# Kernel optimization log

Measured on AMD Instinct MI355X. Metric: run time of the kernel, lower is better.

The kernel has to match this reference:

```python
import jax, jax.numpy as jnp
import numpy as np

B, T, D, E, FF, K = 4, 1024, 1024, 8, 2048, 2
SINKHORN_ITERS = 3


def setup_inputs() -> dict:
    key = jax.random.key(0)
    ks = jax.random.split(key, 7)
    scale = 0.02
    return {
        "x": jax.random.normal(ks[0], (B, T, D), dtype=jnp.float32),
        "router_w": jax.random.normal(ks[1], (E, D), dtype=jnp.float32) * scale,  # nn.Linear(D,E).weight
        "router_b": jnp.zeros((E,), dtype=jnp.float32),
        "temperature": jnp.ones((1,), dtype=jnp.float32) * 0.5,
        "wg": jax.random.normal(ks[2], (E, D, FF), dtype=jnp.float32) * scale,   # expert gate weights
        "wp": jax.random.normal(ks[3], (E, D, FF), dtype=jnp.float32) * scale,   # expert proj weights
        "wo": jax.random.normal(ks[4], (E, FF, D), dtype=jnp.float32) * scale,   # expert out_proj weights
    }


def _sinkhorn(log_alpha, iters=SINKHORN_ITERS):
    for _ in range(iters):
        log_alpha = log_alpha - jax.nn.logsumexp(log_alpha, axis=-1, keepdims=True)
        log_alpha = log_alpha - jax.nn.logsumexp(log_alpha, axis=-2, keepdims=True)
    gates = jnp.exp(log_alpha)
    return gates / (jnp.sum(gates, axis=-1, keepdims=True) + 1e-8)


def reference(x, router_w, router_b, temperature, wg, wp, wo):
    # Router scores with clamped temperature (clamp(min=0.1))
    temp = jnp.maximum(temperature, 0.1)
    scores = (jnp.einsum("btd,ed->bte", x, router_w) + router_b) / temp  # [B,T,E]

    # T>1 and E>1 -> Sinkhorn doubly-stochastic normalization
    gates = _sinkhorn(scores)

    topk_vals, topk_idx = jax.lax.top_k(gates, K)                 # [B,T,K]
    topk_gates = topk_vals / (jnp.sum(topk_vals, axis=-1, keepdims=True) + 1e-8)

    # Dense all-expert FFN (relu-gated GLU), matching mask-and-sum semantics.
    # sum_k sum_i (idx_k==i)*gate_k*expert_i(x) == sum_k gate_k * expert_{idx_k}(x)
    g = jax.nn.relu(jnp.einsum("btd,edf->btef", x, wg))           # [B,T,E,FF]
    p = jnp.einsum("btd,edf->btef", x, wp)                        # [B,T,E,FF]
    all_out = jnp.einsum("btef,efd->bted", g * p, wo)             # [B,T,E,D]

    gathered = jnp.take_along_axis(all_out, topk_idx[..., None], axis=2)  # [B,T,K,D]
    expert_out = jnp.sum(gathered * topk_gates[..., None], axis=2)        # [B,T,D]

    return x + expert_out
```

## Files before the change

kernel.cpp:

```cpp
#include <hip/hip_runtime.h>
#include <hip/hip_bf16.h>
#include <stdint.h>

#define B_   4
#define T_   1024
#define D_   1024
#define E_   8
#define FF_  2048
#define NT_  4096
#define LCAP 9216
#define NT1  (D_ / 32)
#define NT2  (FF_ / 32)

typedef unsigned short u16;
typedef __attribute__((ext_vector_type(8))) short bf16x8;
typedef __attribute__((ext_vector_type(4))) float f32x4;

#define MFMA16(a, b, c) __builtin_amdgcn_mfma_f32_16x16x32_bf16((a), (b), (c), 0, 0, 0)

__device__ __forceinline__ u16 f2bf(float f) {
  union { float f; uint32_t u; } c; c.f = f;
  return (u16)((c.u + 0x7FFFu + ((c.u >> 16) & 1u)) >> 16);
}

__device__ __forceinline__ void gl_lds16(const void* g, void* l) {
  __builtin_amdgcn_global_load_lds(
      (const __attribute__((address_space(1))) uint32_t*)g,
      (__attribute__((address_space(3))) uint32_t*)l, 16, 0, 0);
}


__global__ __launch_bounds__(256) void k_init(int* __restrict__ tok, float* __restrict__ gate,
                                              int* __restrict__ cnt, int* __restrict__ cur) {
  int i = blockIdx.x * 256 + threadIdx.x;
  if (i < LCAP) { tok[i] = 0; gate[i] = 0.f; }
  if (i < E_)   { cnt[i] = 0; cur[i] = 0; }
}

__global__ __launch_bounds__(256) void k_router(const float* __restrict__ x,
                                                const float* __restrict__ rw,
                                                const float* __restrict__ rb,
                                                const float* __restrict__ temp,
                                                float* __restrict__ scores,
                                                float* __restrict__ out,
                                                u16* __restrict__ xb) {
  int wid  = (blockIdx.x * 256 + threadIdx.x) >> 6;
  int lane = threadIdx.x & 63;
  const float* xr = x + (size_t)wid * D_;
  float* orow = out + (size_t)wid * D_;
  u16* xrow = xb + (size_t)wid * D_;
  float acc[E_];
  #pragma unroll
  for (int e = 0; e < E_; ++e) acc[e] = 0.f;
  for (int i = lane; i < D_; i += 64) {
    float xv = xr[i];
    orow[i] = xv;
    xrow[i] = f2bf(xv);
    #pragma unroll
    for (int e = 0; e < E_; ++e) acc[e] += xv * rw[e * D_ + i];
  }
  float inv = 1.0f / fmaxf(temp[0], 0.1f);
  #pragma unroll
  for (int e = 0; e < E_; ++e) {
    float v = acc[e];
    for (int off = 32; off; off >>= 1) v += __shfl_xor(v, off);
    if (lane == 0) scores[(size_t)wid * E_ + e] = (v + rb[e]) * inv;
  }
}

__global__ __launch_bounds__(1024) void k_sinkhorn(const float* __restrict__ scores,
                                                   float* __restrict__ tkg, int* __restrict__ tki,
                                                   int* __restrict__ cnt) {
  const int b = blockIdx.x, t = threadIdx.x;
  const int row = b * T_ + t;
  float s[E_];
  #pragma unroll
  for (int e = 0; e < E_; ++e) s[e] = scores[(size_t)row * E_ + e];

  __shared__ float red[16][E_];
  __shared__ int lcnt[E_];
  if (t < E_) lcnt[t] = 0;
  const int wid = t >> 6, lane = t & 63;

  for (int it = 0; it < 3; ++it) {
    float m = s[0];
    #pragma unroll
    for (int e = 1; e < E_; ++e) m = fmaxf(m, s[e]);
    float sum = 0.f;
    #pragma unroll
    for (int e = 0; e < E_; ++e) sum += expf(s[e] - m);
    float lse = m + logf(sum);
    #pragma unroll
    for (int e = 0; e < E_; ++e) s[e] -= lse;

    float cm[E_];
    #pragma unroll
    for (int e = 0; e < E_; ++e) {
      float v = s[e];
      for (int off = 32; off; off >>= 1) v = fmaxf(v, __shfl_xor(v, off));
      if (lane == 0) red[wid][e] = v;
    }
    __syncthreads();
    #pragma unroll
    for (int e = 0; e < E_; ++e) {
      float mm = red[0][e];
      for (int wv = 1; wv < 16; ++wv) mm = fmaxf(mm, red[wv][e]);
      cm[e] = mm;
    }
    __syncthreads();
    #pragma unroll
    for (int e = 0; e < E_; ++e) {
      float v = expf(s[e] - cm[e]);
      for (int off = 32; off; off >>= 1) v += __shfl_xor(v, off);
      if (lane == 0) red[wid][e] = v;
    }
    __syncthreads();
    #pragma unroll
    for (int e = 0; e < E_; ++e) {
      float ss = 0.f;
      for (int wv = 0; wv < 16; ++wv) ss += red[wv][e];
      s[e] -= cm[e] + logf(ss);
    }
    __syncthreads();
  }

  float g[E_]; float rs = 0.f;
  #pragma unroll
  for (int e = 0; e < E_; ++e) { g[e] = expf(s[e]); rs += g[e]; }
  float inv = 1.f / (rs + 1e-8f);
  #pragma unroll
  for (int e = 0; e < E_; ++e) g[e] *= inv;

  int i0 = 0; float v0 = g[0];
  #pragma unroll
  for (int e = 1; e < E_; ++e) if (g[e] > v0) { v0 = g[e]; i0 = e; }
  int i1 = -1; float v1 = -1e30f;
  #pragma unroll
  for (int e = 0; e < E_; ++e) if (e != i0 && g[e] > v1) { v1 = g[e]; i1 = e; }
  float den = 1.f / (v0 + v1 + 1e-8f);
  tkg[row * 2 + 0] = v0 * den; tki[row * 2 + 0] = i0;
  tkg[row * 2 + 1] = v1 * den; tki[row * 2 + 1] = i1;

  atomicAdd(&lcnt[i0], 1);
  atomicAdd(&lcnt[i1], 1);
  __syncthreads();
  if (t < E_) atomicAdd(&cnt[t], lcnt[t]);
}

__global__ void k_offsets(const int* __restrict__ cnt, int* __restrict__ segoff) {
  if (threadIdx.x == 0 && blockIdx.x == 0) {
    int run = 0;
    for (int e = 0; e < E_; ++e) { segoff[e] = run; run += ((cnt[e] + 127) >> 7) << 7; }
  }
}

__global__ __launch_bounds__(256) void k_scatter(const int* __restrict__ tki, const float* __restrict__ tkg,
                                                 const int* __restrict__ segoff, int* __restrict__ cur,
                                                 int* __restrict__ tok, float* __restrict__ gate) {
  int idx = blockIdx.x * 256 + threadIdx.x;
  int row = idx >> 1;
  int e = tki[idx];
  float g = tkg[idx];
  int pos = atomicAdd(&cur[e], 1);
  int p = segoff[e] + pos;
  tok[p] = row;
  gate[p] = g;
}

__global__ __launch_bounds__(256) void k_transpose(const float* __restrict__ in, u16* __restrict__ out,
                                                   int R, int C) {
  __shared__ __align__(16) u16 t[32][36];
  const size_t msz = (size_t)R * C;
  const float* A = in + blockIdx.z * msz;
  u16* O = out + blockIdx.z * msz;
  const int r0 = blockIdx.y * 32, c0 = blockIdx.x * 32;
  const int tid = threadIdx.x;
  {
    const int i = tid >> 3, j4 = (tid & 7) << 2;
    const float4 v = *(const float4*)(A + (size_t)(r0 + i) * C + c0 + j4);
    ushort4 pk; pk.x = f2bf(v.x); pk.y = f2bf(v.y); pk.z = f2bf(v.z); pk.w = f2bf(v.w);
    *(ushort4*)(&t[i][j4]) = pk;
  }
  __syncthreads();
  {
    const int j2 = tid & 15;
    #pragma unroll
    for (int it = 0; it < 2; ++it) {
      const int r = (tid >> 4) + it * 16;
      uint32_t pv = (uint32_t)t[2 * j2][r] | ((uint32_t)t[2 * j2 + 1][r] << 16);
      *(uint32_t*)(O + (size_t)(c0 + r) * R + r0 + 2 * j2) = pv;
    }
  }
}


__global__ __launch_bounds__(256, 2) void k_stage1(
    const u16* __restrict__ wgT, const u16* __restrict__ wpT,
    const u16* __restrict__ xb, const int* __restrict__ tok,
    const int* __restrict__ cnt, const int* __restrict__ segoff,
    u16* __restrict__ H) {
  const int raw = blockIdx.x;
  const int e   = raw & 7;
  const int rem = raw >> 3;
  const int ft  = rem >> 5;
  const int pt  = rem & 31;
  if (pt * 128 >= cnt[e]) return;
  const int tid = threadIdx.x;
  const int lane = tid & 63;
  const int w = tid >> 6;
  const int lane15 = lane & 15, lchunk = lane >> 4;
  const int fw = w >> 1, pw = w & 1;

  __shared__ __align__(16) u16 LG[3][4096];
  __shared__ __align__(16) u16 LP[3][4096];
  __shared__ __align__(16) u16 LX[3][4096];

  const int prow0 = segoff[e] + pt * 128;
  const size_t wb0 = (size_t)e * FF_ * D_ + (size_t)(ft * 128 + w * 16 + lane15) * D_ + lchunk * 8;
  const size_t wb1 = wb0 + (size_t)64 * D_;
  const u16* gsrc0 = wgT + wb0;  const u16* gsrc1 = wgT + wb1;
  const u16* psrc0 = wpT + wb0;  const u16* psrc1 = wpT + wb1;
  const int tk0 = tok[prow0 + w * 16 + lane15];
  const int tk1 = tok[prow0 + 64 + w * 16 + lane15];
  const u16* xsrc0 = xb + (size_t)tk0 * D_ + lchunk * 8;
  const u16* xsrc1 = xb + (size_t)tk1 * D_ + lchunk * 8;
  const int dst0 = w * 512, dst1 = (w + 4) * 512;

  const f32x4 vz = {0.f, 0.f, 0.f, 0.f};
  f32x4 accG[4][4], accP[4][4];
  #pragma unroll
  for (int m = 0; m < 4; ++m)
    #pragma unroll
    for (int n = 0; n < 4; ++n) { accG[m][n] = vz; accP[m][n] = vz; }

#define ISSUE1(c, t) do { const int o_ = (t) * 32;                 \
    gl_lds16(gsrc0 + o_, &LG[c][dst0]);                            \
    gl_lds16(gsrc1 + o_, &LG[c][dst1]);                            \
    gl_lds16(psrc0 + o_, &LP[c][dst0]);                            \
    gl_lds16(psrc1 + o_, &LP[c][dst1]);                            \
    gl_lds16(xsrc0 + o_, &LX[c][dst0]);                            \
    gl_lds16(xsrc1 + o_, &LX[c][dst1]); } while (0)

#define COMP1(c) do {                                                        \
    const u16* lg = LG[c]; const u16* lp = LP[c]; const u16* lx = LX[c];     \
    bf16x8 ag[4], ap[4], bx[4];                                              \
    _Pragma("unroll")                                                        \
    for (int m = 0; m < 4; ++m) {                                            \
      ag[m] = *(const bf16x8*)(lg + (fw * 4 + m) * 512 + lane * 8);          \
      ap[m] = *(const bf16x8*)(lp + (fw * 4 + m) * 512 + lane * 8);          \
    }                                                                        \
    _Pragma("unroll")                                                        \
    for (int n = 0; n < 4; ++n)                                              \
      bx[n] = *(const bf16x8*)(lx + (pw * 4 + n) * 512 + lane * 8);          \
    __builtin_amdgcn_s_setprio(1);                                           \
    _Pragma("unroll")                                                        \
    for (int m = 0; m < 4; ++m)                                              \
      _Pragma("unroll")                                                      \
      for (int n = 0; n < 4; ++n) {                                          \
        accG[m][n] = MFMA16(ag[m], bx[n], accG[m][n]);                       \
        accP[m][n] = MFMA16(ap[m], bx[n], accP[m][n]);                       \
      }                                                                      \
    __builtin_amdgcn_s_setprio(0); } while (0)

  ISSUE1(0, 0);
  ISSUE1(1, 1);
  #pragma unroll 1
  for (int t = 0; t < NT1 - 1; ++t) {
    asm volatile("s_waitcnt vmcnt(6)" ::: "memory");
    __builtin_amdgcn_s_barrier();
    asm volatile("" ::: "memory");
    if (t + 2 < NT1) { const int cn = (t + 2) % 3; ISSUE1(cn, t + 2); }
    const int c = t % 3;
    COMP1(c);
  }
  asm volatile("s_waitcnt vmcnt(0)" ::: "memory");
  __builtin_amdgcn_s_barrier();
  asm volatile("" ::: "memory");
  COMP1((NT1 - 1) % 3);
#undef ISSUE1
#undef COMP1

  const int jrow = lchunk * 4;
  #pragma unroll
  for (int m = 0; m < 4; ++m) {
    #pragma unroll
    for (int n = 0; n < 4; ++n) {
      union { uint2 v; u16 s[4]; } u;
      #pragma unroll
      for (int j = 0; j < 4; ++j)
        u.s[j] = f2bf(fmaxf(accG[m][n][j], 0.f) * accP[m][n][j]);
      const int prow = prow0 + pw * 64 + n * 16 + lane15;
      const int fcol = ft * 128 + fw * 64 + m * 16 + jrow;
      *(uint2*)(H + (size_t)prow * FF_ + fcol) = u.v;
    }
  }
}

__global__ __launch_bounds__(256, 3) void k_stage2(
    const u16* __restrict__ H, const u16* __restrict__ woT,
    const int* __restrict__ tok, const float* __restrict__ gate,
    const int* __restrict__ cnt, const int* __restrict__ segoff,
    float* __restrict__ out) {
  const int raw = blockIdx.x;
  const int e   = raw & 7;
  const int rem = raw >> 3;
  const int dt  = rem >> 5;
  const int pt  = rem & 31;
  if (pt * 128 >= cnt[e]) return;
  const int tid = threadIdx.x;
  const int lane = tid & 63;
  const int w = tid >> 6;
  const int lane15 = lane & 15, lchunk = lane >> 4;
  const int ph = w >> 1, dh = w & 1;

  __shared__ __align__(16) u16 LH[3][4096];
  __shared__ __align__(16) u16 LW[3][4096];
  __shared__ int   ltok[128];
  __shared__ float lgt[128];

  const int prow0 = segoff[e] + pt * 128;
  if (tid < 128) { ltok[tid] = tok[prow0 + tid]; lgt[tid] = gate[prow0 + tid]; }

  const u16* hsrc0 = H + (size_t)(prow0 + w * 16 + lane15) * FF_ + lchunk * 8;
  const u16* hsrc1 = hsrc0 + (size_t)64 * FF_;
  const u16* wsrc0 = woT + (size_t)e * D_ * FF_
                         + (size_t)(dt * 128 + w * 16 + lane15) * FF_ + lchunk * 8;
  const u16* wsrc1 = wsrc0 + (size_t)64 * FF_;
  const int dst0 = w * 512, dst1 = (w + 4) * 512;

  const f32x4 vz = {0.f, 0.f, 0.f, 0.f};
  f32x4 acc[4][4];
  #pragma unroll
  for (int m = 0; m < 4; ++m)
    #pragma unroll
    for (int n = 0; n < 4; ++n) acc[m][n] = vz;

#define ISSUE2(c, t) do { const int o_ = (t) * 32;                 \
    gl_lds16(hsrc0 + o_, &LH[c][dst0]);                            \
    gl_lds16(hsrc1 + o_, &LH[c][dst1]);                            \
    gl_lds16(wsrc0 + o_, &LW[c][dst0]);                            \
    gl_lds16(wsrc1 + o_, &LW[c][dst1]); } while (0)

#define COMP2(c) do {                                                        \
    const u16* lh = LH[c]; const u16* lw = LW[c];                            \
    bf16x8 ah[4], bw[4];                                                     \
    _Pragma("unroll")                                                        \
    for (int m = 0; m < 4; ++m)                                              \
      ah[m] = *(const bf16x8*)(lh + (ph * 4 + m) * 512 + lane * 8);          \
    _Pragma("unroll")                                                        \
    for (int n = 0; n < 4; ++n)                                              \
      bw[n] = *(const bf16x8*)(lw + (dh * 4 + n) * 512 + lane * 8);          \
    __builtin_amdgcn_s_setprio(1);                                           \
    _Pragma("unroll")                                                        \
    for (int m = 0; m < 4; ++m)                                              \
      _Pragma("unroll")                                                      \
      for (int n = 0; n < 4; ++n)                                            \
        acc[m][n] = MFMA16(ah[m], bw[n], acc[m][n]);                         \
    __builtin_amdgcn_s_setprio(0); } while (0)

  ISSUE2(0, 0);
  ISSUE2(1, 1);
  #pragma unroll 1
  for (int t = 0; t < NT2 - 1; ++t) {
    asm volatile("s_waitcnt vmcnt(4)" ::: "memory");
    __builtin_amdgcn_s_barrier();
    asm volatile("" ::: "memory");
    if (t + 2 < NT2) { const int cn = (t + 2) % 3; ISSUE2(cn, t + 2); }
    const int c = t % 3;
    COMP2(c);
  }
  asm volatile("s_waitcnt vmcnt(0)" ::: "memory");
  __builtin_amdgcn_s_barrier();
  asm volatile("" ::: "memory");
  COMP2((NT2 - 1) % 3);
#undef ISSUE2
#undef COMP2

  const int jrow = lchunk * 4;
  #pragma unroll
  for (int m = 0; m < 4; ++m) {
    #pragma unroll
    for (int n = 0; n < 4; ++n) {
      const int dcol = dt * 128 + dh * 64 + n * 16 + lane15;
      #pragma unroll
      for (int j = 0; j < 4; ++j) {
        const int pl = ph * 64 + m * 16 + jrow + j;
        unsafeAtomicAdd(&out[(size_t)ltok[pl] * D_ + dcol], lgt[pl] * acc[m][n][j]);
      }
    }
  }
}


extern "C" void kernel_launch(void* const* d_in, const int* in_sizes, int n_in,
                              void* d_out, int out_size, void* d_ws, size_t ws_size,
                              hipStream_t stream) {
  const float* x    = (const float*)d_in[0];
  const float* rw   = (const float*)d_in[1];
  const float* rb   = (const float*)d_in[2];
  const float* temp = (const float*)d_in[3];
  const float* wg   = (const float*)d_in[4];
  const float* wp   = (const float*)d_in[5];
  const float* wo   = (const float*)d_in[6];
  float* out = (float*)d_out;
  char* ws = (char*)d_ws;

  const size_t O_XB  = 0;
  const size_t O_WGT = 8388608;
  const size_t O_WPT = O_WGT + 33554432;
  const size_t O_WOT = O_WGT;
  const size_t O_H   = O_WPT + 33554432;
  const size_t O_SC  = O_H + (size_t)LCAP * FF_ * 2;
  const size_t O_TKG = O_SC + (size_t)NT_ * E_ * 4;
  const size_t O_TKI = O_TKG + (size_t)NT_ * 2 * 4;
  const size_t O_CNT = O_TKI + (size_t)NT_ * 2 * 4;
  const size_t O_CUR = O_CNT + 128;
  const size_t O_SEG = O_CUR + 128;
  const size_t O_TOK = O_SEG + 128;
  const size_t O_GTE = O_TOK + (size_t)LCAP * 4;
  const size_t REQ   = O_GTE + (size_t)LCAP * 4;
  if (ws_size < REQ) return;

  u16*   xb     = (u16*)(ws + O_XB);
  u16*   wgT    = (u16*)(ws + O_WGT);
  u16*   wpT    = (u16*)(ws + O_WPT);
  u16*   woT    = (u16*)(ws + O_WOT);
  u16*   Hbuf   = (u16*)(ws + O_H);
  float* scores = (float*)(ws + O_SC);
  float* tkg    = (float*)(ws + O_TKG);
  int*   tki    = (int*)(ws + O_TKI);
  int*   cnt    = (int*)(ws + O_CNT);
  int*   cur    = (int*)(ws + O_CUR);
  int*   segoff = (int*)(ws + O_SEG);
  int*   tok    = (int*)(ws + O_TOK);
  float* gate   = (float*)(ws + O_GTE);

  k_init<<<(LCAP + 255) / 256, 256, 0, stream>>>(tok, gate, cnt, cur);
  k_router<<<NT_ / 4, 256, 0, stream>>>(x, rw, rb, temp, scores, out, xb);
  k_sinkhorn<<<B_, 1024, 0, stream>>>(scores, tkg, tki, cnt);
  k_offsets<<<1, 64, 0, stream>>>(cnt, segoff);
  k_scatter<<<(NT_ * 2) / 256, 256, 0, stream>>>(tki, tkg, segoff, cur, tok, gate);

  k_transpose<<<dim3(FF_ / 32, D_ / 32, E_), 256, 0, stream>>>(wg, wgT, D_, FF_);
  k_transpose<<<dim3(FF_ / 32, D_ / 32, E_), 256, 0, stream>>>(wp, wpT, D_, FF_);

  k_stage1<<<32 * 16 * E_, 256, 0, stream>>>(wgT, wpT, xb, tok, cnt, segoff, Hbuf);

  k_transpose<<<dim3(D_ / 32, FF_ / 32, E_), 256, 0, stream>>>(wo, woT, FF_, D_);

  k_stage2<<<32 * 8 * E_, 256, 0, stream>>>(Hbuf, woT, tok, gate, cnt, segoff, out);
}
```

Before: 479.7 us.

## Replace LDS-staged GEMM pipelines with direct global-to-register double buffering

Both expert GEMM kernels drop their triple-buffered global_load_lds shared-memory staging and barriers. Each wave now loads its MFMA operands straight from global memory into registers, double-buffered across k-steps. Stage 1 shrinks its per-block F tile from 128 to 64 (grid doubled) and interleaves gate/proj rows in one accumulator set, raising occupancy to 3 blocks per CU. This removes LDS traffic and barrier stalls, but loses cross-wave operand sharing, so each wave issues redundant global loads and relies on the cache for reuse.

```diff
diff --git a/kernel.cpp b/kernel.cpp
--- a/kernel.cpp
+++ b/kernel.cpp
@@ -21,12 +21,6 @@
 __device__ __forceinline__ u16 f2bf(float f) {
   union { float f; uint32_t u; } c; c.f = f;
   return (u16)((c.u + 0x7FFFu + ((c.u >> 16) & 1u)) >> 16);
-}
-
-__device__ __forceinline__ void gl_lds16(const void* g, void* l) {
-  __builtin_amdgcn_global_load_lds(
-      (const __attribute__((address_space(1))) uint32_t*)g,
-      (__attribute__((address_space(3))) uint32_t*)l, 16, 0, 0);
 }
 
 
@@ -194,7 +188,7 @@
 }
 
 
-__global__ __launch_bounds__(256, 2) void k_stage1(
+__global__ __launch_bounds__(256, 3) void k_stage1(
     const u16* __restrict__ wgT, const u16* __restrict__ wpT,
     const u16* __restrict__ xb, const int* __restrict__ tok,
     const int* __restrict__ cnt, const int* __restrict__ segoff,
@@ -205,92 +199,73 @@
   const int ft  = rem >> 5;
   const int pt  = rem & 31;
   if (pt * 128 >= cnt[e]) return;
-  const int tid = threadIdx.x;
-  const int lane = tid & 63;
-  const int w = tid >> 6;
-  const int lane15 = lane & 15, lchunk = lane >> 4;
+  const int lane = threadIdx.x & 63;
+  const int w = threadIdx.x >> 6;
   const int fw = w >> 1, pw = w & 1;
-
-  __shared__ __align__(16) u16 LG[3][4096];
-  __shared__ __align__(16) u16 LP[3][4096];
-  __shared__ __align__(16) u16 LX[3][4096];
-
-  const int prow0 = segoff[e] + pt * 128;
-  const size_t wb0 = (size_t)e * FF_ * D_ + (size_t)(ft * 128 + w * 16 + lane15) * D_ + lchunk * 8;
-  const size_t wb1 = wb0 + (size_t)64 * D_;
-  const u16* gsrc0 = wgT + wb0;  const u16* gsrc1 = wgT + wb1;
-  const u16* psrc0 = wpT + wb0;  const u16* psrc1 = wpT + wb1;
-  const int tk0 = tok[prow0 + w * 16 + lane15];
-  const int tk1 = tok[prow0 + 64 + w * 16 + lane15];
-  const u16* xsrc0 = xb + (size_t)tk0 * D_ + lchunk * 8;
-  const u16* xsrc1 = xb + (size_t)tk1 * D_ + lchunk * 8;
-  const int dst0 = w * 512, dst1 = (w + 4) * 512;
+  const int lane15 = lane & 15, lk8 = (lane >> 4) * 8;
+
+  const int prow0 = segoff[e] + pt * 128 + pw * 64;
+  const int fbase = ft * 64 + fw * 32;
+
+  const u16* ga0; const u16* ga1; const u16* pa0; const u16* pa1;
+  {
+    size_t r0 = (size_t)e * FF_ * D_ + (size_t)(fbase + lane15) * D_ + lk8;
+    size_t r1 = r0 + (size_t)16 * D_;
+    ga0 = wgT + r0; ga1 = wgT + r1; pa0 = wpT + r0; pa1 = wpT + r1;
+  }
+  const u16* bx0 = xb + (size_t)tok[prow0 +  0 + lane15] * D_ + lk8;
+  const u16* bx1 = xb + (size_t)tok[prow0 + 16 + lane15] * D_ + lk8;
+  const u16* bx2 = xb + (size_t)tok[prow0 + 32 + lane15] * D_ + lk8;
+  const u16* bx3 = xb + (size_t)tok[prow0 + 48 + lane15] * D_ + lk8;
 
   const f32x4 vz = {0.f, 0.f, 0.f, 0.f};
-  f32x4 accG[4][4], accP[4][4];
+  f32x4 acc[4][4];
   #pragma unroll
   for (int m = 0; m < 4; ++m)
     #pragma unroll
-    for (int n = 0; n < 4; ++n) { accG[m][n] = vz; accP[m][n] = vz; }
-
-#define ISSUE1(c, t) do { const int o_ = (t) * 32;                 \
-    gl_lds16(gsrc0 + o_, &LG[c][dst0]);                            \
-    gl_lds16(gsrc1 + o_, &LG[c][dst1]);                            \
-    gl_lds16(psrc0 + o_, &LP[c][dst0]);                            \
-    gl_lds16(psrc1 + o_, &LP[c][dst1]);                            \
-    gl_lds16(xsrc0 + o_, &LX[c][dst0]);                            \
-    gl_lds16(xsrc1 + o_, &LX[c][dst1]); } while (0)
-
-#define COMP1(c) do {                                                        \
-    const u16* lg = LG[c]; const u16* lp = LP[c]; const u16* lx = LX[c];     \
-    bf16x8 ag[4], ap[4], bx[4];                                              \
-    _Pragma("unroll")                                                        \
-    for (int m = 0; m < 4; ++m) {                                            \
-      ag[m] = *(const bf16x8*)(lg + (fw * 4 + m) * 512 + lane * 8);          \
-      ap[m] = *(const bf16x8*)(lp + (fw * 4 + m) * 512 + lane * 8);          \
-    }                                                                        \
-    _Pragma("unroll")                                                        \
-    for (int n = 0; n < 4; ++n)                                              \
-      bx[n] = *(const bf16x8*)(lx + (pw * 4 + n) * 512 + lane * 8);          \
-    __builtin_amdgcn_s_setprio(1);                                           \
-    _Pragma("unroll")                                                        \
-    for (int m = 0; m < 4; ++m)                                              \
-      _Pragma("unroll")                                                      \
-      for (int n = 0; n < 4; ++n) {                                          \
-        accG[m][n] = MFMA16(ag[m], bx[n], accG[m][n]);                       \
-        accP[m][n] = MFMA16(ap[m], bx[n], accP[m][n]);                       \
-      }                                                                      \
-    __builtin_amdgcn_s_setprio(0); } while (0)
-
-  ISSUE1(0, 0);
-  ISSUE1(1, 1);
+    for (int n = 0; n < 4; ++n) acc[m][n] = vz;
+
+  bf16x8 A0[4], B0[4], A1[4], B1[4];
+
+#define LD1(AS, BS, t) do { const int o_ = (t) * 32;                \
+    AS[0] = *(const bf16x8*)(ga0 + o_);                             \
+    AS[1] = *(const bf16x8*)(pa0 + o_);                             \
+    AS[2] = *(const bf16x8*)(ga1 + o_);                             \
+    AS[3] = *(const bf16x8*)(pa1 + o_);                             \
+    BS[0] = *(const bf16x8*)(bx0 + o_);                             \
+    BS[1] = *(const bf16x8*)(bx1 + o_);                             \
+    BS[2] = *(const bf16x8*)(bx2 + o_);                             \
+    BS[3] = *(const bf16x8*)(bx3 + o_); } while (0)
+
+#define FM1(AS, BS) do {                                            \
+    _Pragma("unroll")                                               \
+    for (int m = 0; m < 4; ++m)                                     \
+      _Pragma("unroll")                                             \
+      for (int n = 0; n < 4; ++n)                                   \
+        acc[m][n] = MFMA16(AS[m], BS[n], acc[m][n]); } while (0)
+
+  LD1(A0, B0, 0);
   #pragma unroll 1
-  for (int t = 0; t < NT1 - 1; ++t) {
-    asm volatile("s_waitcnt vmcnt(6)" ::: "memory");
-    __builtin_amdgcn_s_barrier();
-    asm volatile("" ::: "memory");
-    if (t + 2 < NT1) { const int cn = (t + 2) % 3; ISSUE1(cn, t + 2); }
-    const int c = t % 3;
-    COMP1(c);
-  }
-  asm volatile("s_waitcnt vmcnt(0)" ::: "memory");
-  __builtin_amdgcn_s_barrier();
-  asm volatile("" ::: "memory");
-  COMP1((NT1 - 1) % 3);
-#undef ISSUE1
-#undef COMP1
-
-  const int jrow = lchunk * 4;
-  #pragma unroll
-  for (int m = 0; m < 4; ++m) {
+  for (int t = 0; t < NT1; t += 2) {
+    LD1(A1, B1, t + 1);
+    FM1(A0, B0);
+    if (t + 2 < NT1) LD1(A0, B0, t + 2);
+    FM1(A1, B1);
+  }
+#undef LD1
+#undef FM1
+
+  const int jrow = (lane >> 4) * 4;
+  #pragma unroll
+  for (int q = 0; q < 2; ++q) {
+    const int fcol = fbase + q * 16 + jrow;
     #pragma unroll
     for (int n = 0; n < 4; ++n) {
+      const int prow = prow0 + n * 16 + lane15;
       union { uint2 v; u16 s[4]; } u;
       #pragma unroll
       for (int j = 0; j < 4; ++j)
-        u.s[j] = f2bf(fmaxf(accG[m][n][j], 0.f) * accP[m][n][j]);
-      const int prow = prow0 + pw * 64 + n * 16 + lane15;
-      const int fcol = ft * 128 + fw * 64 + m * 16 + jrow;
+        u.s[j] = f2bf(fmaxf(acc[2 * q][n][j], 0.f) * acc[2 * q + 1][n][j]);
       *(uint2*)(H + (size_t)prow * FF_ + fcol) = u.v;
     }
   }
@@ -307,26 +282,23 @@
   const int dt  = rem >> 5;
   const int pt  = rem & 31;
   if (pt * 128 >= cnt[e]) return;
-  const int tid = threadIdx.x;
-  const int lane = tid & 63;
-  const int w = tid >> 6;
-  const int lane15 = lane & 15, lchunk = lane >> 4;
-  const int ph = w >> 1, dh = w & 1;
-
-  __shared__ __align__(16) u16 LH[3][4096];
-  __shared__ __align__(16) u16 LW[3][4096];
-  __shared__ int   ltok[128];
-  __shared__ float lgt[128];
-
-  const int prow0 = segoff[e] + pt * 128;
-  if (tid < 128) { ltok[tid] = tok[prow0 + tid]; lgt[tid] = gate[prow0 + tid]; }
-
-  const u16* hsrc0 = H + (size_t)(prow0 + w * 16 + lane15) * FF_ + lchunk * 8;
-  const u16* hsrc1 = hsrc0 + (size_t)64 * FF_;
-  const u16* wsrc0 = woT + (size_t)e * D_ * FF_
-                         + (size_t)(dt * 128 + w * 16 + lane15) * FF_ + lchunk * 8;
-  const u16* wsrc1 = wsrc0 + (size_t)64 * FF_;
-  const int dst0 = w * 512, dst1 = (w + 4) * 512;
+  const int lane = threadIdx.x & 63;
+  const int w = threadIdx.x >> 6;
+  const int pw = w >> 1, dw = w & 1;
+  const int lane15 = lane & 15, lk8 = (lane >> 4) * 8;
+
+  const int p0 = segoff[e] + pt * 128 + pw * 64;
+  const int d0 = dt * 128 + dw * 64;
+
+  const u16* ha0 = H + (size_t)(p0 +  0 + lane15) * FF_ + lk8;
+  const u16* ha1 = H + (size_t)(p0 + 16 + lane15) * FF_ + lk8;
+  const u16* ha2 = H + (size_t)(p0 + 32 + lane15) * FF_ + lk8;
+  const u16* ha3 = H + (size_t)(p0 + 48 + lane15) * FF_ + lk8;
+  const size_t wbase = (size_t)e * D_ * FF_;
+  const u16* wa0 = woT + wbase + (size_t)(d0 +  0 + lane15) * FF_ + lk8;
+  const u16* wa1 = woT + wbase + (size_t)(d0 + 16 + lane15) * FF_ + lk8;
+  const u16* wa2 = woT + wbase + (size_t)(d0 + 32 + lane15) * FF_ + lk8;
+  const u16* wa3 = woT + wbase + (size_t)(d0 + 48 + lane15) * FF_ + lk8;
 
   const f32x4 vz = {0.f, 0.f, 0.f, 0.f};
   f32x4 acc[4][4];
@@ -335,57 +307,48 @@
     #pragma unroll
     for (int n = 0; n < 4; ++n) acc[m][n] = vz;
 
-#define ISSUE2(c, t) do { const int o_ = (t) * 32;                 \
-    gl_lds16(hsrc0 + o_, &LH[c][dst0]);                            \
-    gl_lds16(hsrc1 + o_, &LH[c][dst1]);                            \
-    gl_lds16(wsrc0 + o_, &LW[c][dst0]);                            \
-    gl_lds16(wsrc1 + o_, &LW[c][dst1]); } while (0)
-
-#define COMP2(c) do {                                                        \
-    const u16* lh = LH[c]; const u16* lw = LW[c];                            \
-    bf16x8 ah[4], bw[4];                                                     \
-    _Pragma("unroll")                                                        \
-    for (int m = 0; m < 4; ++m)                                              \
-      ah[m] = *(const bf16x8*)(lh + (ph * 4 + m) * 512 + lane * 8);          \
-    _Pragma("unroll")                                                        \
-    for (int n = 0; n < 4; ++n)                                              \
-      bw[n] = *(const bf16x8*)(lw + (dh * 4 + n) * 512 + lane * 8);          \
-    __builtin_amdgcn_s_setprio(1);                                           \
-    _Pragma("unroll")                                                        \
-    for (int m = 0; m < 4; ++m)                                              \
-      _Pragma("unroll")                                                      \
-      for (int n = 0; n < 4; ++n)                                            \
-        acc[m][n] = MFMA16(ah[m], bw[n], acc[m][n]);                         \
-    __builtin_amdgcn_s_setprio(0); } while (0)
-
-  ISSUE2(0, 0);
-  ISSUE2(1, 1);
+  bf16x8 A0[4], B0[4], A1[4], B1[4];
+
+#define LD2(AS, BS, t) do { const int o_ = (t) * 32;                \
+    AS[0] = *(const bf16x8*)(ha0 + o_);                             \
+    AS[1] = *(const bf16x8*)(ha1 + o_);                             \
+    AS[2] = *(const bf16x8*)(ha2 + o_);                             \
+    AS[3] = *(const bf16x8*)(ha3 + o_);                             \
+    BS[0] = *(const bf16x8*)(wa0 + o_);                             \
+    BS[1] = *(const bf16x8*)(wa1 + o_);                             \
+    BS[2] = *(const bf16x8*)(wa2 + o_);                             \
+    BS[3] = *(const bf16x8*)(wa3 + o_); } while (0)
+
+#define FM2(AS, BS) do {                                            \
+    _Pragma("unroll")                                               \
+    for (int m = 0; m < 4; ++m)                                     \
+      _Pragma("unroll")                                             \
+      for (int n = 0; n < 4; ++n)                                   \
+        acc[m][n] = MFMA16(AS[m], BS[n], acc[m][n]); } while (0)
+
+  LD2(A0, B0, 0);
   #pragma unroll 1
-  for (int t = 0; t < NT2 - 1; ++t) {
-    asm volatile("s_waitcnt vmcnt(4)" ::: "memory");
-    __builtin_amdgcn_s_barrier();
-    asm volatile("" ::: "memory");
-    if (t + 2 < NT2) { const int cn = (t + 2) % 3; ISSUE2(cn, t + 2); }
-    const int c = t % 3;
-    COMP2(c);
-  }
-  asm volatile("s_waitcnt vmcnt(0)" ::: "memory");
-  __builtin_amdgcn_s_barrier();
-  asm volatile("" ::: "memory");
-  COMP2((NT2 - 1) % 3);
-#undef ISSUE2
-#undef COMP2
-
-  const int jrow = lchunk * 4;
+  for (int t = 0; t < NT2; t += 2) {
+    LD2(A1, B1, t + 1);
+    FM2(A0, B0);
+    if (t + 2 < NT2) LD2(A0, B0, t + 2);
+    FM2(A1, B1);
+  }
+#undef LD2
+#undef FM2
+
+  const int jrow = (lane >> 4) * 4;
   #pragma unroll
   for (int m = 0; m < 4; ++m) {
     #pragma unroll
-    for (int n = 0; n < 4; ++n) {
-      const int dcol = dt * 128 + dh * 64 + n * 16 + lane15;
+    for (int j = 0; j < 4; ++j) {
+      const int prow = p0 + m * 16 + jrow + j;
+      const int tk = tok[prow];
+      const float gt = gate[prow];
       #pragma unroll
-      for (int j = 0; j < 4; ++j) {
-        const int pl = ph * 64 + m * 16 + jrow + j;
-        unsafeAtomicAdd(&out[(size_t)ltok[pl] * D_ + dcol], lgt[pl] * acc[m][n][j]);
+      for (int n = 0; n < 4; ++n) {
+        const int dcol = d0 + n * 16 + lane15;
+        unsafeAtomicAdd(&out[(size_t)tk * D_ + dcol], gt * acc[m][n][j]);
       }
     }
   }
@@ -444,7 +407,7 @@
   k_transpose<<<dim3(FF_ / 32, D_ / 32, E_), 256, 0, stream>>>(wg, wgT, D_, FF_);
   k_transpose<<<dim3(FF_ / 32, D_ / 32, E_), 256, 0, stream>>>(wp, wpT, D_, FF_);
 
-  k_stage1<<<32 * 16 * E_, 256, 0, stream>>>(wgT, wpT, xb, tok, cnt, segoff, Hbuf);
+  k_stage1<<<32 * 32 * E_, 256, 0, stream>>>(wgT, wpT, xb, tok, cnt, segoff, Hbuf);
 
   k_transpose<<<dim3(D_ / 32, FF_ / 32, E_), 256, 0, stream>>>(wo, woT, FF_, D_);
 
```

Result: slower. 743.7 us (+55.0%).
